# Performance work log

Measured on AMD Instinct MI355X. Metric: run time of the kernel, lower is better.

## Reference

```python
import jax, jax.numpy as jnp
import numpy as np

D = 768
OUT = 196
EPS = 1e-6


def setup_inputs() -> dict:
    key = jax.random.key(0)
    k_x, k_w, k_b, k_g, k_beta = jax.random.split(key, 5)
    x = jax.random.normal(k_x, (16, 4096, D), dtype=jnp.float32)
    # LayerNorm affine params
    gamma = jnp.ones((D,), dtype=jnp.float32) + 0.01 * jax.random.normal(k_g, (D,), dtype=jnp.float32)
    beta = 0.01 * jax.random.normal(k_beta, (D,), dtype=jnp.float32)
    # Linear params (torch default init: U(-1/sqrt(D), 1/sqrt(D)))
    bound = 1.0 / np.sqrt(D)
    W = jax.random.uniform(k_w, (OUT, D), minval=-bound, maxval=bound, dtype=jnp.float32)
    b = jax.random.uniform(k_b, (OUT,), minval=-bound, maxval=bound, dtype=jnp.float32)
    return {"x": x, "gamma": gamma, "beta": beta, "W": W, "b": b}


def reference(x, gamma, beta, W, b):
    # LayerNorm over last dim (768), eps=1e-6, elementwise affine
    mean = jnp.mean(x, axis=-1, keepdims=True)
    var = jnp.mean(jnp.square(x - mean), axis=-1, keepdims=True)
    xn = (x - mean) * jax.lax.rsqrt(var + EPS) * gamma + beta
    # Linear 768 -> 196
    return jnp.einsum('bsd,od->bso', xn, W) + b
```

## Files before the change

### kernel.cpp

```cpp
#include <hip/hip_runtime.h>

#define DD   768
#define OUTN 196
#define NT   13
#define KT   24

typedef __attribute__((ext_vector_type(8))) _Float16 halfx8;
typedef __attribute__((ext_vector_type(4))) float    f32x4;

__global__ __launch_bounds__(256) void wprep_kernel(
    const float* __restrict__ W, const float* __restrict__ gamma,
    const float* __restrict__ beta, const float* __restrict__ bias,
    _Float16* __restrict__ Wh, float* __restrict__ Ssum, float* __restrict__ cvec)
{
    __shared__ float red[2][4];
    const int n   = blockIdx.x;
    const int tid = threadIdx.x;
    float s1 = 0.f, s2 = 0.f;
#pragma unroll
    for (int kk = 0; kk < 3; ++kk) {
        const int k = tid + kk * 256;
        const float w = W[n * DD + k];
        const _Float16 h = (_Float16)(w * gamma[k]);
        Wh[n * DD + k] = h;
        s1 += (float)h;
        s2 += beta[k] * w;
    }
#pragma unroll
    for (int off = 32; off > 0; off >>= 1) {
        s1 += __shfl_xor(s1, off);
        s2 += __shfl_xor(s2, off);
    }
    if ((tid & 63) == 0) { red[0][tid >> 6] = s1; red[1][tid >> 6] = s2; }
    __syncthreads();
    if (tid == 0) {
        Ssum[n] = red[0][0] + red[0][1] + red[0][2] + red[0][3];
        cvec[n] = bias[n] + red[1][0] + red[1][1] + red[1][2] + red[1][3];
    }
}

__global__ __launch_bounds__(256, 4) void fused_ln_linear(
    const float* __restrict__ x, const _Float16* __restrict__ Wh,
    const float* __restrict__ Ssum, const float* __restrict__ cvec,
    float* __restrict__ out)
{
    const int tid  = threadIdx.x;
    const int wv   = tid >> 6;
    const int lane = tid & 63;
    const int ln16 = lane & 15;
    const int q    = lane >> 4;

    const long row0 = (long)blockIdx.x * 64 + wv * 16;
    const float* xp = x + (row0 + ln16) * DD + q * 8;

    int woff[NT];
#pragma unroll
    for (int nt = 0; nt < NT; ++nt) {
        int n = nt * 16 + ln16;
        if (n >= OUTN) n = OUTN - 1;
        woff[nt] = n * DD + q * 8;
    }

    f32x4 acc[NT];
#pragma unroll
    for (int i = 0; i < NT; ++i) acc[i] = (f32x4){0.f, 0.f, 0.f, 0.f};

    float s = 0.f, ss = 0.f;

#pragma unroll 2
    for (int kt = 0; kt < KT; ++kt) {
        const float4 v0 = *(const float4*)(xp + kt * 32);
        const float4 v1 = *(const float4*)(xp + kt * 32 + 4);
        s  += v0.x + v0.y + v0.z + v0.w + v1.x + v1.y + v1.z + v1.w;
        ss += v0.x * v0.x + v0.y * v0.y + v0.z * v0.z + v0.w * v0.w
            + v1.x * v1.x + v1.y * v1.y + v1.z * v1.z + v1.w * v1.w;
        halfx8 hi, lo;
        hi[0] = (_Float16)v0.x; lo[0] = (_Float16)(v0.x - (float)hi[0]);
        hi[1] = (_Float16)v0.y; lo[1] = (_Float16)(v0.y - (float)hi[1]);
        hi[2] = (_Float16)v0.z; lo[2] = (_Float16)(v0.z - (float)hi[2]);
        hi[3] = (_Float16)v0.w; lo[3] = (_Float16)(v0.w - (float)hi[3]);
        hi[4] = (_Float16)v1.x; lo[4] = (_Float16)(v1.x - (float)hi[4]);
        hi[5] = (_Float16)v1.y; lo[5] = (_Float16)(v1.y - (float)hi[5]);
        hi[6] = (_Float16)v1.z; lo[6] = (_Float16)(v1.z - (float)hi[6]);
        hi[7] = (_Float16)v1.w; lo[7] = (_Float16)(v1.w - (float)hi[7]);
#pragma unroll
        for (int nt = 0; nt < NT; ++nt) {
            const halfx8 bw = *(const halfx8*)(Wh + woff[nt] + kt * 32);
            acc[nt] = __builtin_amdgcn_mfma_f32_16x16x32_f16(hi, bw, acc[nt], 0, 0, 0);
            acc[nt] = __builtin_amdgcn_mfma_f32_16x16x32_f16(lo, bw, acc[nt], 0, 0, 0);
        }
    }

    s  += __shfl_xor(s, 16);  s  += __shfl_xor(s, 32);
    ss += __shfl_xor(ss, 16); ss += __shfl_xor(ss, 32);
    const float mean_r = s * (1.f / DD);
    const float rstd_r = rsqrtf(ss * (1.f / DD) - mean_r * mean_r + 1e-6f);

    float mb[4], rb[4];
#pragma unroll
    for (int rg = 0; rg < 4; ++rg) {
        const int src = q * 4 + rg;
        mb[rg] = __shfl(mean_r, src);
        rb[rg] = __shfl(rstd_r, src);
    }

    const long obase = (row0 + q * 4) * OUTN;
#pragma unroll
    for (int nt = 0; nt < NT; ++nt) {
        const int n = nt * 16 + ln16;
        if (n < OUTN) {
            const float Sp = Ssum[n];
            const float cn = cvec[n];
#pragma unroll
            for (int rg = 0; rg < 4; ++rg)
                out[obase + rg * OUTN + n] = rb[rg] * (acc[nt][rg] - mb[rg] * Sp) + cn;
        }
    }
}

extern "C" void kernel_launch(void* const* d_in, const int* in_sizes, int n_in,
                              void* d_out, int out_size, void* d_ws, size_t ws_size,
                              hipStream_t stream) {
    const float* x     = (const float*)d_in[0];
    const float* gamma = (const float*)d_in[1];
    const float* beta  = (const float*)d_in[2];
    const float* W     = (const float*)d_in[3];
    const float* b     = (const float*)d_in[4];
    float* out = (float*)d_out;

    _Float16* Wh  = (_Float16*)d_ws;
    float*    Ss  = (float*)((char*)d_ws + OUTN * DD * sizeof(_Float16));
    float*    cv  = Ss + OUTN;

    wprep_kernel<<<OUTN, 256, 0, stream>>>(W, gamma, beta, b, Wh, Ss, cv);

    const long rows = 16L * 4096;
    fused_ln_linear<<<rows / 64, 256, 0, stream>>>(x, Wh, Ss, cv, out);
}
```

Before: 414.9 us.

## Stage W tiles in swizzled LDS and split output columns across three blocks

```diff
diff --git a/kernel.cpp b/kernel.cpp
--- a/kernel.cpp
+++ b/kernel.cpp
@@ -1,9 +1,8 @@
 #include <hip/hip_runtime.h>
 
-#define DD   768
-#define OUTN 196
-#define NT   13
-#define KT   24
+#define DD    768
+#define OUTN  196
+#define NSLOT 96
 
 typedef __attribute__((ext_vector_type(8))) _Float16 halfx8;
 typedef __attribute__((ext_vector_type(4))) float    f32x4;
@@ -39,41 +38,53 @@
     }
 }
 
-__global__ __launch_bounds__(256, 4) void fused_ln_linear(
+template <int T, int N0, int PR>
+__device__ __forceinline__ void run_part(
     const float* __restrict__ x, const _Float16* __restrict__ Wh,
     const float* __restrict__ Ssum, const float* __restrict__ cvec,
-    float* __restrict__ out)
+    float* __restrict__ out, _Float16* ldsW, int mblk)
 {
-    const int tid  = threadIdx.x;
+    const int tid = threadIdx.x;
+
+    for (int ci = tid; ci < NSLOT * PR; ci += 1024) {
+        const int r  = ci / NSLOT;
+        const int sl = ci - r * NSLOT;
+        int nrow = N0 + r;
+        if (nrow > OUTN - 1) nrow = OUTN - 1;
+        const halfx8 w = *(const halfx8*)(Wh + nrow * DD + sl * 8);
+        *(halfx8*)(ldsW + (r * NSLOT + (sl ^ (r & 7))) * 8) = w;
+    }
+    __syncthreads();
+
     const int wv   = tid >> 6;
     const int lane = tid & 63;
     const int ln16 = lane & 15;
     const int q    = lane >> 4;
+    const int rx   = ln16 & 7;
 
-    const long row0 = (long)blockIdx.x * 64 + wv * 16;
+    const long row0 = (long)mblk * 256 + wv * 16;
     const float* xp = x + (row0 + ln16) * DD + q * 8;
 
-    int woff[NT];
+    int rbase[T];
 #pragma unroll
-    for (int nt = 0; nt < NT; ++nt) {
-        int n = nt * 16 + ln16;
-        if (n >= OUTN) n = OUTN - 1;
-        woff[nt] = n * DD + q * 8;
-    }
+    for (int t = 0; t < T; ++t) rbase[t] = (t * 16 + ln16) * DD;
 
-    f32x4 acc[NT];
+    f32x4 acc[T];
 #pragma unroll
-    for (int i = 0; i < NT; ++i) acc[i] = (f32x4){0.f, 0.f, 0.f, 0.f};
+    for (int t = 0; t < T; ++t) acc[t] = (f32x4){0.f, 0.f, 0.f, 0.f};
 
     float s = 0.f, ss = 0.f;
 
-#pragma unroll 2
-    for (int kt = 0; kt < KT; ++kt) {
+#pragma unroll
+    for (int kt = 0; kt < 24; ++kt) {
         const float4 v0 = *(const float4*)(xp + kt * 32);
         const float4 v1 = *(const float4*)(xp + kt * 32 + 4);
-        s  += v0.x + v0.y + v0.z + v0.w + v1.x + v1.y + v1.z + v1.w;
-        ss += v0.x * v0.x + v0.y * v0.y + v0.z * v0.z + v0.w * v0.w
-            + v1.x * v1.x + v1.y * v1.y + v1.z * v1.z + v1.w * v1.w;
+        s  += (v0.x + v0.y) + (v0.z + v0.w) + (v1.x + v1.y) + (v1.z + v1.w);
+        ss  = fmaf(v0.x, v0.x, ss); ss = fmaf(v0.y, v0.y, ss);
+        ss  = fmaf(v0.z, v0.z, ss); ss = fmaf(v0.w, v0.w, ss);
+        ss  = fmaf(v1.x, v1.x, ss); ss = fmaf(v1.y, v1.y, ss);
+        ss  = fmaf(v1.z, v1.z, ss); ss = fmaf(v1.w, v1.w, ss);
+
         halfx8 hi, lo;
         hi[0] = (_Float16)v0.x; lo[0] = (_Float16)(v0.x - (float)hi[0]);
         hi[1] = (_Float16)v0.y; lo[1] = (_Float16)(v0.y - (float)hi[1]);
@@ -83,11 +94,13 @@
         hi[5] = (_Float16)v1.y; lo[5] = (_Float16)(v1.y - (float)hi[5]);
         hi[6] = (_Float16)v1.z; lo[6] = (_Float16)(v1.z - (float)hi[6]);
         hi[7] = (_Float16)v1.w; lo[7] = (_Float16)(v1.w - (float)hi[7]);
+
 #pragma unroll
-        for (int nt = 0; nt < NT; ++nt) {
-            const halfx8 bw = *(const halfx8*)(Wh + woff[nt] + kt * 32);
-            acc[nt] = __builtin_amdgcn_mfma_f32_16x16x32_f16(hi, bw, acc[nt], 0, 0, 0);
-            acc[nt] = __builtin_amdgcn_mfma_f32_16x16x32_f16(lo, bw, acc[nt], 0, 0, 0);
+        for (int t = 0; t < T; ++t) {
+            const int slot = (kt * 4 + q) ^ rx;
+            const halfx8 bw = *(const halfx8*)(ldsW + rbase[t] + slot * 8);
+            acc[t] = __builtin_amdgcn_mfma_f32_16x16x32_f16(hi, bw, acc[t], 0, 0, 0);
+            acc[t] = __builtin_amdgcn_mfma_f32_16x16x32_f16(lo, bw, acc[t], 0, 0, 0);
         }
     }
 
@@ -99,23 +112,35 @@
     float mb[4], rb[4];
 #pragma unroll
     for (int rg = 0; rg < 4; ++rg) {
-        const int src = q * 4 + rg;
-        mb[rg] = __shfl(mean_r, src);
-        rb[rg] = __shfl(rstd_r, src);
+        mb[rg] = __shfl(mean_r, q * 4 + rg);
+        rb[rg] = __shfl(rstd_r, q * 4 + rg);
     }
 
     const long obase = (row0 + q * 4) * OUTN;
 #pragma unroll
-    for (int nt = 0; nt < NT; ++nt) {
-        const int n = nt * 16 + ln16;
+    for (int t = 0; t < T; ++t) {
+        const int n = N0 + t * 16 + ln16;
         if (n < OUTN) {
             const float Sp = Ssum[n];
             const float cn = cvec[n];
 #pragma unroll
             for (int rg = 0; rg < 4; ++rg)
-                out[obase + rg * OUTN + n] = rb[rg] * (acc[nt][rg] - mb[rg] * Sp) + cn;
+                out[obase + rg * OUTN + n] = rb[rg] * (acc[t][rg] - mb[rg] * Sp) + cn;
         }
     }
+}
+
+__global__ __launch_bounds__(1024, 4) void fused_ln_linear(
+    const float* __restrict__ x, const _Float16* __restrict__ Wh,
+    const float* __restrict__ Ssum, const float* __restrict__ cvec,
+    float* __restrict__ out)
+{
+    __shared__ _Float16 ldsW[80 * NSLOT * 8];
+    const int part = blockIdx.x % 3;
+    const int m    = blockIdx.x / 3;
+    if (part == 0)      run_part<5,   0, 80>(x, Wh, Ssum, cvec, out, ldsW, m);
+    else if (part == 1) run_part<4,  80, 64>(x, Wh, Ssum, cvec, out, ldsW, m);
+    else                run_part<4, 144, 64>(x, Wh, Ssum, cvec, out, ldsW, m);
 }
 
 extern "C" void kernel_launch(void* const* d_in, const int* in_sizes, int n_in,
@@ -128,12 +153,11 @@
     const float* b     = (const float*)d_in[4];
     float* out = (float*)d_out;
 
-    _Float16* Wh  = (_Float16*)d_ws;
-    float*    Ss  = (float*)((char*)d_ws + OUTN * DD * sizeof(_Float16));
-    float*    cv  = Ss + OUTN;
+    _Float16* Wh = (_Float16*)d_ws;
+    float*    Ss = (float*)((char*)d_ws + OUTN * DD * sizeof(_Float16));
+    float*    cv = Ss + OUTN;
 
     wprep_kernel<<<OUTN, 256, 0, stream>>>(W, gamma, beta, b, Wh, Ss, cv);
 
-    const long rows = 16L * 4096;
-    fused_ln_linear<<<rows / 64, 256, 0, stream>>>(x, Wh, Ss, cv, out);
+    fused_ln_linear<<<256 * 3, 1024, 0, stream>>>(x, Wh, Ss, cv, out);
 }
```

After: 348.0 us. -16.1%, faster.
